# Kernel optimization log

Hardware: AMD Instinct MI355X
Metric: run time of the kernel (lower is better)

## Reference

```python
import jax, jax.numpy as jnp
import numpy as np

B, L, D, N_ORIG, GD, K_TARGET = 8, 512, 1024, 8192, 64, 256
_PI, _PJ = np.triu_indices(L, k=1)  # all global pairs i<j, shared across batch


def setup_inputs() -> dict:
    key = jax.random.key(0)
    k1, k2, k3 = jax.random.split(key, 3)
    x = jax.random.normal(k1, (B, L, D), jnp.float32)
    source = jax.random.uniform(k2, (B, L, N_ORIG), jnp.float32)
    W = jax.random.normal(k3, (GD, D), jnp.float32) * 0.02  # group_proj weight (out,in), no bias
    return {"x": x, "source": source, "W": W, "target_len": K_TARGET}


def _merge_single(x, s, W, r_step, pi, pj):
    # x: (S,D), s: (S,N). One greedy global merge step (r_step = S//2 >= r_total).
    S = x.shape[0]
    g = x @ W.T                                   # (S, GD)
    gn = jnp.linalg.norm(g, axis=-1)              # token weights (g.norm)
    gu = g / jnp.maximum(gn, 1e-12)[:, None]      # F.normalize(g, dim=-1)
    sim = (gu[pi] * gu[pj]).sum(-1)               # (P,) cosine sim of each pair
    # deterministic order: (-sim, i, j); lexsort's last key is primary
    order = jnp.lexsort((pj, pi, -sim))
    si = pi[order]
    sj = pj[order]

    # sequential greedy disjoint (mutual-exclusion) selection
    def body(carry, ij):
        partner, isj, cnt = carry
        i, j = ij
        used_i = (partner[i] >= 0) | isj[i]
        used_j = (partner[j] >= 0) | isj[j]
        sel = (~used_i) & (~used_j) & (cnt < r_step)
        partner = partner.at[i].set(jnp.where(sel, j, partner[i]))
        isj = isj.at[j].set(isj[j] | sel)
        return (partner, isj, cnt + sel.astype(jnp.int32)), None

    init = (jnp.full((S,), -1, jnp.int32), jnp.zeros((S,), bool), jnp.int32(0))
    (partner, isj, _), _ = jax.lax.scan(body, init, (si, sj))

    # kept tokens (everything not a merged-away j), in original order; greedy on a
    # complete graph always selects exactly r_step pairs, so K = S - r_step is static
    K = S - r_step
    keep = jnp.argsort(isj.astype(jnp.int32), stable=True)[:K]  # (K,)
    pk = partner[keep]
    has_p = pk >= 0
    pjx = jnp.where(has_p, pk, keep)  # safe partner index
    wi = gn[keep]
    wj = gn[pjx]
    tot = wi + wj + 1e-8
    xm = jnp.where(has_p[:, None], (wi[:, None] * x[keep] + wj[:, None] * x[pjx]) / tot[:, None], x[keep])
    sm = jnp.where(has_p[:, None], s[keep] + s[pjx], s[keep])
    return xm, sm


def reference(x, source, W, target_len):
    Bb, Ll, Dd = x.shape
    r_total = Ll - target_len
    if r_total <= 0:
        return x, source
    # with target_len = L//2, r_total <= floor(L/2): single greedy step (faithful)
    r_step = min(r_total, Ll // 2)
    pi = jnp.asarray(_PI, jnp.int32)
    pj = jnp.asarray(_PJ, jnp.int32)
    f = lambda xb, sb: _merge_single(xb, sb, W, r_step, pi, pj)
    return jax.vmap(f)(x, source)
```

## Files before the change

### kernel.cpp

```cpp
#include <hip/hip_runtime.h>

#define B_ 8
#define L_ 512
#define D_ 1024
#define N_ 8192
#define GD_ 64
#define K_ 256

__global__ __launch_bounds__(256) void wt_kernel(const float* __restrict__ W,
                                                 float* __restrict__ Wt) {
  int idx = blockIdx.x * 256 + threadIdx.x;
  int d = idx >> 6, g = idx & 63;
  Wt[idx] = W[(size_t)g * D_ + d];
}

__global__ __launch_bounds__(256) void gproj_kernel(const float* __restrict__ x,
                                                    const float* __restrict__ Wt,
                                                    float* __restrict__ gu,
                                                    float* __restrict__ gn) {
  const int KC = 128;
  __shared__ float xs[16][KC];
  __shared__ float wsT[GD_][KC + 4];
  int blk = blockIdx.x;
  int b = blk >> 5;
  int t0 = (blk & 31) * 16;
  int tid = threadIdx.x;
  int dg = tid & 15, tg = tid >> 4;
  const float* xb = x + ((size_t)b * L_ + t0) * D_;
  float ax[4] = {0, 0, 0, 0}, ay[4] = {0, 0, 0, 0};
  float az[4] = {0, 0, 0, 0}, aw[4] = {0, 0, 0, 0};
  for (int kc = 0; kc < D_; kc += KC) {
    for (int f = tid; f < 16 * KC / 4; f += 256) {
      int t = f >> 5, k4 = f & 31;
      *(float4*)&xs[t][k4 * 4] = *(const float4*)(xb + (size_t)t * D_ + kc + k4 * 4);
    }
    for (int f = tid; f < GD_ * KC; f += 256) {
      int kk = f >> 6, d = f & 63;
      wsT[d][kk] = Wt[(size_t)(kc + kk) * GD_ + d];
    }
    __syncthreads();
#pragma unroll 4
    for (int kk = 0; kk < KC; kk += 4) {
      float4 xv = *(const float4*)&xs[tg][kk];
#pragma unroll
      for (int dd = 0; dd < 4; ++dd) {
        float4 wv = *(const float4*)&wsT[dg * 4 + dd][kk];
        ax[dd] += xv.x * wv.x;
        ay[dd] += xv.y * wv.y;
        az[dd] += xv.z * wv.z;
        aw[dd] += xv.w * wv.w;
      }
    }
    __syncthreads();
  }
  float g[4];
  double ss = 0.0;
#pragma unroll
  for (int dd = 0; dd < 4; ++dd) {
    g[dd] = (ax[dd] + ay[dd]) + (az[dd] + aw[dd]);
    ss += (double)g[dd] * (double)g[dd];
  }
#pragma unroll
  for (int off = 1; off < 16; off <<= 1) ss += __shfl_xor(ss, off);
  float gnv = (float)sqrt(ss);
  float dn = fmaxf(gnv, 1e-12f);
  int t = t0 + tg;
  if (dg == 0) gn[(size_t)b * L_ + t] = gnv;
  float* gup = gu + ((size_t)b * L_ + t) * GD_ + dg * 4;
#pragma unroll
  for (int dd = 0; dd < 4; ++dd) gup[dd] = g[dd] / dn;
}

__global__ __launch_bounds__(256) void sim_kernel(const float* __restrict__ gu,
                                                  float* __restrict__ simo) {
  __shared__ __align__(16) float A[32][65];
  __shared__ __align__(16) float BsT[64][36];
  int b = blockIdx.z;
  int i0 = blockIdx.y * 32, j0 = blockIdx.x * 32;
  const float* gb = gu + (size_t)b * L_ * GD_;
  int tid = threadIdx.x;
  for (int f = tid; f < 32 * GD_; f += 256) {
    int r = f >> 6, k = f & 63;
    A[r][k] = gb[(size_t)(i0 + r) * GD_ + k];
    BsT[k][r] = gb[(size_t)(j0 + r) * GD_ + k];
  }
  __syncthreads();
  int r = tid >> 3, c4 = (tid & 7) * 4;
  double a0 = 0, a1 = 0, a2 = 0, a3 = 0;
#pragma unroll 8
  for (int k = 0; k < GD_; ++k) {
    double a = (double)A[r][k];
    float4 bv = *(const float4*)&BsT[k][c4];
    a0 += a * (double)bv.x;
    a1 += a * (double)bv.y;
    a2 += a * (double)bv.z;
    a3 += a * (double)bv.w;
  }
  float4 o;
  o.x = (float)a0; o.y = (float)a1; o.z = (float)a2; o.w = (float)a3;
  *(float4*)(simo + (size_t)b * L_ * L_ + (size_t)(i0 + r) * L_ + (j0 + c4)) = o;
}

__global__ __launch_bounds__(256) void topk_kernel(const float* __restrict__ sim,
                                                   unsigned long long* __restrict__ cand) {
  int wid = blockIdx.x * 4 + (threadIdx.x >> 6);
  int b = wid >> 9;
  int a = wid & 511;
  int lane = threadIdx.x & 63;
  const float* row = sim + ((size_t)b * L_ + a) * L_;
  int c0 = lane * 8;
  float4 v0 = *(const float4*)(row + c0);
  float4 v1 = *(const float4*)(row + c0 + 4);
  float vv[8] = {v0.x, v0.y, v0.z, v0.w, v1.x, v1.y, v1.z, v1.w};
  unsigned long long k[8];
#pragma unroll
  for (int s = 0; s < 8; ++s) {
    int bb = c0 + s;
    if (bb == a) {
      k[s] = 0;
    } else {
      unsigned u = __float_as_uint(vv[s]);
      u = (u & 0x80000000u) ? ~u : (u | 0x80000000u);
      int i = a < bb ? a : bb, j = a < bb ? bb : a;
      k[s] = ((unsigned long long)u << 18) |
             (unsigned long long)(0x3FFFFu - (((unsigned)i << 9) | (unsigned)j));
    }
  }
  unsigned long long* out = cand + ((size_t)b * L_ + a) * 16;
#pragma unroll
  for (int pass = 0; pass < 16; ++pass) {
    unsigned long long m = k[0];
#pragma unroll
    for (int s = 1; s < 8; ++s) m = k[s] > m ? k[s] : m;
#pragma unroll
    for (int off = 32; off; off >>= 1) {
      unsigned long long o = __shfl_xor(m, off);
      if (o > m) m = o;
    }
#pragma unroll
    for (int s = 0; s < 8; ++s)
      if (k[s] == m) k[s] = 0;
    if (lane == 0) out[pass] = m;
  }
}

__global__ __launch_bounds__(512) void match_kernel(const float* __restrict__ sim,
                                                    const unsigned long long* __restrict__ cand,
                                                    int* __restrict__ keepI,
                                                    int* __restrict__ keepJ) {
  int b = blockIdx.x;
  const float* S = sim + (size_t)b * L_ * L_;
  const unsigned long long* C = cand + (size_t)b * L_ * 16;
  __shared__ unsigned long long bestkey[L_];
  __shared__ short partner[L_];
  __shared__ short liveList[L_], liveTmp[L_], rescanQ[L_];
  __shared__ unsigned char liveF[L_], needs[L_], head[L_];
  __shared__ int nLiveS, nLiveNew, nQ;
  int tid = threadIdx.x;
  int wave = tid >> 6, lane = tid & 63;
  if (tid < L_) {
    partner[tid] = -1;
    liveF[tid] = 1;
    needs[tid] = 1;
    head[tid] = 0;
    liveList[tid] = (short)tid;
    bestkey[tid] = 0ull;
  }
  if (tid == 0) nLiveS = L_;
  __syncthreads();
  for (int round = 0; round < 300; ++round) {
    int nLive = nLiveS;
    if (nLive == 0) break;
    if (tid == 0) nQ = 0;
    __syncthreads();
    for (int idx = tid; idx < nLive; idx += 512) {
      int a = liveList[idx];
      if (needs[a]) {
        int h = head[a];
        unsigned long long bk = 0ull;
        while (h < 16) {
          unsigned long long key = C[a * 16 + h];
          if (key) {
            unsigned pk = 0x3FFFFu - (unsigned)(key & 0x3FFFFull);
            int i = (int)(pk >> 9), j = (int)(pk & 511u);
            int p = (i == a) ? j : i;
            if (liveF[p]) { bk = key; break; }
          }
          ++h;
        }
        head[a] = (unsigned char)h;
        if (bk) {
          bestkey[a] = bk;
          needs[a] = 0;
        } else {
          int q = atomicAdd(&nQ, 1);
          rescanQ[q] = (short)a;
        }
      }
    }
    __syncthreads();
    int nq = nQ;
    for (int q = wave; q < nq; q += 8) {
      int a = rescanQ[q];
      unsigned long long mk = 0ull;
      for (int kk = lane; kk < nLive; kk += 64) {
        int bb = liveList[kk];
        if (bb != a) {
          float sv = S[(size_t)a * L_ + bb];
          unsigned u = __float_as_uint(sv);
          u = (u & 0x80000000u) ? ~u : (u | 0x80000000u);
          int i = a < bb ? a : bb, j = a < bb ? bb : a;
          unsigned long long key =
              ((unsigned long long)u << 18) |
              (unsigned long long)(0x3FFFFu - (((unsigned)i << 9) | (unsigned)j));
          if (key > mk) mk = key;
        }
      }
#pragma unroll
      for (int off = 32; off; off >>= 1) {
        unsigned long long o = __shfl_xor(mk, off);
        if (o > mk) mk = o;
      }
      if (lane == 0) {
        bestkey[a] = mk;
        needs[a] = 0;
      }
    }
    __syncthreads();
    for (int idx = tid; idx < nLive; idx += 512) {
      int a = liveList[idx];
      unsigned pk = 0x3FFFFu - (unsigned)(bestkey[a] & 0x3FFFFull);
      int i = (int)(pk >> 9), j = (int)(pk & 511u);
      int p = (i == a) ? j : i;
      unsigned pk2 = 0x3FFFFu - (unsigned)(bestkey[p] & 0x3FFFFull);
      int i2 = (int)(pk2 >> 9), j2 = (int)(pk2 & 511u);
      int p2 = (i2 == p) ? j2 : i2;
      if (p2 == a) {
        partner[a] = (short)p;
        liveF[a] = 0;
      }
    }
    __syncthreads();
    if (tid == 0) nLiveNew = 0;
    __syncthreads();
    for (int idx = tid; idx < nLive; idx += 512) {
      int a = liveList[idx];
      if (liveF[a]) {
        unsigned pk = 0x3FFFFu - (unsigned)(bestkey[a] & 0x3FFFFull);
        int i = (int)(pk >> 9), j = (int)(pk & 511u);
        int p = (i == a) ? j : i;
        if (!liveF[p]) needs[a] = 1;
        int pos = atomicAdd(&nLiveNew, 1);
        liveTmp[pos] = (short)a;
      }
    }
    __syncthreads();
    int nNew = nLiveNew;
    for (int idx = tid; idx < nNew; idx += 512) liveList[idx] = liveTmp[idx];
    if (tid == 0) nLiveS = nNew;
    __syncthreads();
  }
  if (wave == 0) {
    int base = 0;
    for (int c = 0; c < 8; ++c) {
      int a = c * 64 + lane;
      bool kept = partner[a] > a;
      unsigned long long m = __ballot(kept);
      int pos = base + (int)__popcll(m & ((1ull << lane) - 1ull));
      if (kept) {
        keepI[b * K_ + pos] = a;
        keepJ[b * K_ + pos] = partner[a];
      }
      base += (int)__popcll(m);
    }
  }
}

__global__ __launch_bounds__(256) void mergex_kernel(const float* __restrict__ x,
                                                     const float* __restrict__ gn,
                                                     const int* __restrict__ keepI,
                                                     const int* __restrict__ keepJ,
                                                     float* __restrict__ out) {
  int row = blockIdx.x;
  int b = row >> 8;
  int i = keepI[row], j = keepJ[row];
  float wi = gn[(size_t)b * L_ + i], wj = gn[(size_t)b * L_ + j];
  float tot = wi + wj + 1e-8f;
  const float4* xi = (const float4*)(x + ((size_t)b * L_ + i) * D_);
  const float4* xj = (const float4*)(x + ((size_t)b * L_ + j) * D_);
  float4* o = (float4*)(out + (size_t)row * D_);
  int t = threadIdx.x;
  float4 a = xi[t], c = xj[t];
  float4 r;
  r.x = (wi * a.x + wj * c.x) / tot;
  r.y = (wi * a.y + wj * c.y) / tot;
  r.z = (wi * a.z + wj * c.z) / tot;
  r.w = (wi * a.w + wj * c.w) / tot;
  o[t] = r;
}

__global__ __launch_bounds__(256) void merges_kernel(const float* __restrict__ s,
                                                     const int* __restrict__ keepI,
                                                     const int* __restrict__ keepJ,
                                                     float* __restrict__ out) {
  int row = blockIdx.x;
  int b = row >> 8;
  int i = keepI[row], j = keepJ[row];
  const float4* si = (const float4*)(s + ((size_t)b * L_ + i) * N_);
  const float4* sj = (const float4*)(s + ((size_t)b * L_ + j) * N_);
  float4* o = (float4*)(out + (size_t)row * N_);
  for (int t = threadIdx.x; t < N_ / 4; t += 256) {
    float4 a = si[t], c = sj[t];
    float4 r;
    r.x = a.x + c.x;
    r.y = a.y + c.y;
    r.z = a.z + c.z;
    r.w = a.w + c.w;
    o[t] = r;
  }
}

extern "C" void kernel_launch(void* const* d_in, const int* in_sizes, int n_in,
                              void* d_out, int out_size, void* d_ws, size_t ws_size,
                              hipStream_t stream) {
  (void)in_sizes; (void)n_in; (void)out_size; (void)ws_size;
  const float* x = (const float*)d_in[0];
  const float* src = (const float*)d_in[1];
  const float* W = (const float*)d_in[2];

  float* ws = (float*)d_ws;
  float* Wt = ws;
  float* gu = Wt + 65536;
  float* gn = gu + (size_t)B_ * L_ * GD_;
  float* sim = gn + (size_t)B_ * L_;
  int* keepI = (int*)(sim + (size_t)B_ * L_ * L_);
  int* keepJ = keepI + B_ * K_;
  unsigned long long* cand = (unsigned long long*)(keepJ + B_ * K_);

  float* xm = (float*)d_out;
  float* sm = xm + (size_t)B_ * K_ * D_;

  wt_kernel<<<256, 256, 0, stream>>>(W, Wt);
  gproj_kernel<<<256, 256, 0, stream>>>(x, Wt, gu, gn);
  sim_kernel<<<dim3(16, 16, 8), 256, 0, stream>>>(gu, sim);
  topk_kernel<<<1024, 256, 0, stream>>>(sim, cand);
  match_kernel<<<B_, 512, 0, stream>>>(sim, cand, keepI, keepJ);
  mergex_kernel<<<B_ * K_, 256, 0, stream>>>(x, gn, keepI, keepJ, xm);
  merges_kernel<<<B_ * K_, 256, 0, stream>>>(src, keepI, keepJ, sm);
}
```

Baseline: 355.1 us.

## Drop W transpose kernel, fuse merge kernels, stage candidates in LDS

Removes the separate W-transpose kernel and loads W rows directly with float4 in gproj, which now uses 128 threads each computing two tokens. The sim kernel keeps the A row in registers instead of LDS. The match kernel copies the candidate lists into shared memory, ping-pongs the live lists to drop a copy loop, and removes two barriers per round. The x and source merge kernels are fused into one launch. Together these aim to cut launch count, global-memory latency in the serial matching loop, and synchronisation, at the cost of more LDS in match_kernel and fewer threads in gproj.

```diff
diff --git a/kernel.cpp b/kernel.cpp
--- a/kernel.cpp
+++ b/kernel.cpp
@@ -7,89 +7,97 @@
 #define GD_ 64
 #define K_ 256
 
-__global__ __launch_bounds__(256) void wt_kernel(const float* __restrict__ W,
-                                                 float* __restrict__ Wt) {
-  int idx = blockIdx.x * 256 + threadIdx.x;
-  int d = idx >> 6, g = idx & 63;
-  Wt[idx] = W[(size_t)g * D_ + d];
-}
-
-__global__ __launch_bounds__(256) void gproj_kernel(const float* __restrict__ x,
-                                                    const float* __restrict__ Wt,
+__global__ __launch_bounds__(128) void gproj_kernel(const float* __restrict__ x,
+                                                    const float* __restrict__ W,
                                                     float* __restrict__ gu,
                                                     float* __restrict__ gn) {
   const int KC = 128;
-  __shared__ float xs[16][KC];
-  __shared__ float wsT[GD_][KC + 4];
+  __shared__ __align__(16) float xs[16][KC];
+  __shared__ __align__(16) float wsT[GD_][KC + 4];
   int blk = blockIdx.x;
   int b = blk >> 5;
   int t0 = (blk & 31) * 16;
   int tid = threadIdx.x;
   int dg = tid & 15, tg = tid >> 4;
   const float* xb = x + ((size_t)b * L_ + t0) * D_;
-  float ax[4] = {0, 0, 0, 0}, ay[4] = {0, 0, 0, 0};
-  float az[4] = {0, 0, 0, 0}, aw[4] = {0, 0, 0, 0};
+  float acc[2][4][4];
+#pragma unroll
+  for (int tk = 0; tk < 2; ++tk)
+#pragma unroll
+    for (int dd = 0; dd < 4; ++dd)
+#pragma unroll
+      for (int c = 0; c < 4; ++c) acc[tk][dd][c] = 0.f;
   for (int kc = 0; kc < D_; kc += KC) {
-    for (int f = tid; f < 16 * KC / 4; f += 256) {
+    for (int f = tid; f < 16 * KC / 4; f += 128) {
       int t = f >> 5, k4 = f & 31;
       *(float4*)&xs[t][k4 * 4] = *(const float4*)(xb + (size_t)t * D_ + kc + k4 * 4);
     }
-    for (int f = tid; f < GD_ * KC; f += 256) {
-      int kk = f >> 6, d = f & 63;
-      wsT[d][kk] = Wt[(size_t)(kc + kk) * GD_ + d];
+    for (int f = tid; f < GD_ * KC / 4; f += 128) {
+      int d = f >> 5, k4 = f & 31;
+      *(float4*)&wsT[d][k4 * 4] = *(const float4*)(W + (size_t)d * D_ + kc + k4 * 4);
     }
     __syncthreads();
 #pragma unroll 4
     for (int kk = 0; kk < KC; kk += 4) {
-      float4 xv = *(const float4*)&xs[tg][kk];
+      float4 xv0 = *(const float4*)&xs[tg][kk];
+      float4 xv1 = *(const float4*)&xs[tg + 8][kk];
 #pragma unroll
       for (int dd = 0; dd < 4; ++dd) {
         float4 wv = *(const float4*)&wsT[dg * 4 + dd][kk];
-        ax[dd] += xv.x * wv.x;
-        ay[dd] += xv.y * wv.y;
-        az[dd] += xv.z * wv.z;
-        aw[dd] += xv.w * wv.w;
-      }
-    }
-    __syncthreads();
-  }
-  float g[4];
-  double ss = 0.0;
-#pragma unroll
-  for (int dd = 0; dd < 4; ++dd) {
-    g[dd] = (ax[dd] + ay[dd]) + (az[dd] + aw[dd]);
-    ss += (double)g[dd] * (double)g[dd];
-  }
-#pragma unroll
-  for (int off = 1; off < 16; off <<= 1) ss += __shfl_xor(ss, off);
-  float gnv = (float)sqrt(ss);
-  float dn = fmaxf(gnv, 1e-12f);
-  int t = t0 + tg;
-  if (dg == 0) gn[(size_t)b * L_ + t] = gnv;
-  float* gup = gu + ((size_t)b * L_ + t) * GD_ + dg * 4;
-#pragma unroll
-  for (int dd = 0; dd < 4; ++dd) gup[dd] = g[dd] / dn;
+        acc[0][dd][0] += xv0.x * wv.x;
+        acc[0][dd][1] += xv0.y * wv.y;
+        acc[0][dd][2] += xv0.z * wv.z;
+        acc[0][dd][3] += xv0.w * wv.w;
+        acc[1][dd][0] += xv1.x * wv.x;
+        acc[1][dd][1] += xv1.y * wv.y;
+        acc[1][dd][2] += xv1.z * wv.z;
+        acc[1][dd][3] += xv1.w * wv.w;
+      }
+    }
+    __syncthreads();
+  }
+#pragma unroll
+  for (int tk = 0; tk < 2; ++tk) {
+    float g[4];
+    double ss = 0.0;
+#pragma unroll
+    for (int dd = 0; dd < 4; ++dd) {
+      g[dd] = (acc[tk][dd][0] + acc[tk][dd][1]) + (acc[tk][dd][2] + acc[tk][dd][3]);
+      ss += (double)g[dd] * (double)g[dd];
+    }
+#pragma unroll
+    for (int off = 1; off < 16; off <<= 1) ss += __shfl_xor(ss, off);
+    float gnv = (float)sqrt(ss);
+    float dn = fmaxf(gnv, 1e-12f);
+    int t = t0 + tg + tk * 8;
+    if (dg == 0) gn[(size_t)b * L_ + t] = gnv;
+    float* gup = gu + ((size_t)b * L_ + t) * GD_ + dg * 4;
+#pragma unroll
+    for (int dd = 0; dd < 4; ++dd) gup[dd] = g[dd] / dn;
+  }
 }
 
 __global__ __launch_bounds__(256) void sim_kernel(const float* __restrict__ gu,
                                                   float* __restrict__ simo) {
-  __shared__ __align__(16) float A[32][65];
-  __shared__ __align__(16) float BsT[64][36];
+  __shared__ __align__(16) float BsT[GD_][36];
   int b = blockIdx.z;
   int i0 = blockIdx.y * 32, j0 = blockIdx.x * 32;
   const float* gb = gu + (size_t)b * L_ * GD_;
   int tid = threadIdx.x;
   for (int f = tid; f < 32 * GD_; f += 256) {
     int r = f >> 6, k = f & 63;
-    A[r][k] = gb[(size_t)(i0 + r) * GD_ + k];
     BsT[k][r] = gb[(size_t)(j0 + r) * GD_ + k];
   }
+  int r = tid >> 3, c4 = (tid & 7) * 4;
+  float af[GD_];
+  const float4* arow = (const float4*)(gb + (size_t)(i0 + r) * GD_);
+#pragma unroll
+  for (int q = 0; q < 16; ++q) *(float4*)&af[q * 4] = arow[q];
   __syncthreads();
-  int r = tid >> 3, c4 = (tid & 7) * 4;
   double a0 = 0, a1 = 0, a2 = 0, a3 = 0;
-#pragma unroll 8
+#pragma unroll
   for (int k = 0; k < GD_; ++k) {
-    double a = (double)A[r][k];
+    double a = (double)af[k];
     float4 bv = *(const float4*)&BsT[k][c4];
     a0 += a * (double)bv.x;
     a1 += a * (double)bv.y;
@@ -151,35 +159,41 @@
   int b = blockIdx.x;
   const float* S = sim + (size_t)b * L_ * L_;
   const unsigned long long* C = cand + (size_t)b * L_ * 16;
+  __shared__ unsigned long long candL[L_][16];
   __shared__ unsigned long long bestkey[L_];
   __shared__ short partner[L_];
-  __shared__ short liveList[L_], liveTmp[L_], rescanQ[L_];
+  __shared__ short liveA[L_], liveB[L_], rescanQ[L_];
   __shared__ unsigned char liveF[L_], needs[L_], head[L_];
-  __shared__ int nLiveS, nLiveNew, nQ;
+  __shared__ int nLiveNew, nQ;
   int tid = threadIdx.x;
   int wave = tid >> 6, lane = tid & 63;
+  for (int f = tid; f < L_ * 8; f += 512)
+    ((ulonglong2*)candL)[f] = ((const ulonglong2*)C)[f];
   if (tid < L_) {
     partner[tid] = -1;
     liveF[tid] = 1;
     needs[tid] = 1;
     head[tid] = 0;
-    liveList[tid] = (short)tid;
+    liveA[tid] = (short)tid;
     bestkey[tid] = 0ull;
   }
-  if (tid == 0) nLiveS = L_;
+  if (tid == 0) {
+    nLiveNew = L_;
+    nQ = 0;
+  }
   __syncthreads();
   for (int round = 0; round < 300; ++round) {
-    int nLive = nLiveS;
+    int nLive = nLiveNew;
     if (nLive == 0) break;
-    if (tid == 0) nQ = 0;
-    __syncthreads();
+    short* cur = (round & 1) ? liveB : liveA;
+    short* nxt = (round & 1) ? liveA : liveB;
     for (int idx = tid; idx < nLive; idx += 512) {
-      int a = liveList[idx];
+      int a = cur[idx];
       if (needs[a]) {
         int h = head[a];
         unsigned long long bk = 0ull;
         while (h < 16) {
-          unsigned long long key = C[a * 16 + h];
+          unsigned long long key = candL[a][h];
           if (key) {
             unsigned pk = 0x3FFFFu - (unsigned)(key & 0x3FFFFull);
             int i = (int)(pk >> 9), j = (int)(pk & 511u);
@@ -204,7 +218,7 @@
       int a = rescanQ[q];
       unsigned long long mk = 0ull;
       for (int kk = lane; kk < nLive; kk += 64) {
-        int bb = liveList[kk];
+        int bb = cur[kk];
         if (bb != a) {
           float sv = S[(size_t)a * L_ + bb];
           unsigned u = __float_as_uint(sv);
@@ -226,9 +240,10 @@
         needs[a] = 0;
       }
     }
+    if (tid == 0) nLiveNew = 0;
     __syncthreads();
     for (int idx = tid; idx < nLive; idx += 512) {
-      int a = liveList[idx];
+      int a = cur[idx];
       unsigned pk = 0x3FFFFu - (unsigned)(bestkey[a] & 0x3FFFFull);
       int i = (int)(pk >> 9), j = (int)(pk & 511u);
       int p = (i == a) ? j : i;
@@ -241,23 +256,18 @@
       }
     }
     __syncthreads();
-    if (tid == 0) nLiveNew = 0;
-    __syncthreads();
     for (int idx = tid; idx < nLive; idx += 512) {
-      int a = liveList[idx];
+      int a = cur[idx];
       if (liveF[a]) {
         unsigned pk = 0x3FFFFu - (unsigned)(bestkey[a] & 0x3FFFFull);
         int i = (int)(pk >> 9), j = (int)(pk & 511u);
         int p = (i == a) ? j : i;
         if (!liveF[p]) needs[a] = 1;
         int pos = atomicAdd(&nLiveNew, 1);
-        liveTmp[pos] = (short)a;
-      }
-    }
-    __syncthreads();
-    int nNew = nLiveNew;
-    for (int idx = tid; idx < nNew; idx += 512) liveList[idx] = liveTmp[idx];
-    if (tid == 0) nLiveS = nNew;
+        nxt[pos] = (short)a;
+      }
+    }
+    if (tid == 0) nQ = 0;
     __syncthreads();
   }
   if (wave == 0) {
@@ -276,47 +286,44 @@
   }
 }
 
-__global__ __launch_bounds__(256) void mergex_kernel(const float* __restrict__ x,
-                                                     const float* __restrict__ gn,
-                                                     const int* __restrict__ keepI,
-                                                     const int* __restrict__ keepJ,
-                                                     float* __restrict__ out) {
+__global__ __launch_bounds__(256) void merge_kernel(const float* __restrict__ x,
+                                                    const float* __restrict__ s,
+                                                    const float* __restrict__ gn,
+                                                    const int* __restrict__ keepI,
+                                                    const int* __restrict__ keepJ,
+                                                    float* __restrict__ xm,
+                                                    float* __restrict__ sm) {
   int row = blockIdx.x;
   int b = row >> 8;
   int i = keepI[row], j = keepJ[row];
   float wi = gn[(size_t)b * L_ + i], wj = gn[(size_t)b * L_ + j];
   float tot = wi + wj + 1e-8f;
-  const float4* xi = (const float4*)(x + ((size_t)b * L_ + i) * D_);
-  const float4* xj = (const float4*)(x + ((size_t)b * L_ + j) * D_);
-  float4* o = (float4*)(out + (size_t)row * D_);
   int t = threadIdx.x;
-  float4 a = xi[t], c = xj[t];
-  float4 r;
-  r.x = (wi * a.x + wj * c.x) / tot;
-  r.y = (wi * a.y + wj * c.y) / tot;
-  r.z = (wi * a.z + wj * c.z) / tot;
-  r.w = (wi * a.w + wj * c.w) / tot;
-  o[t] = r;
-}
-
-__global__ __launch_bounds__(256) void merges_kernel(const float* __restrict__ s,
-                                                     const int* __restrict__ keepI,
-                                                     const int* __restrict__ keepJ,
-                                                     float* __restrict__ out) {
-  int row = blockIdx.x;
-  int b = row >> 8;
-  int i = keepI[row], j = keepJ[row];
-  const float4* si = (const float4*)(s + ((size_t)b * L_ + i) * N_);
-  const float4* sj = (const float4*)(s + ((size_t)b * L_ + j) * N_);
-  float4* o = (float4*)(out + (size_t)row * N_);
-  for (int t = threadIdx.x; t < N_ / 4; t += 256) {
-    float4 a = si[t], c = sj[t];
+  {
+    const float4* xi = (const float4*)(x + ((size_t)b * L_ + i) * D_);
+    const float4* xj = (const float4*)(x + ((size_t)b * L_ + j) * D_);
+    float4* o = (float4*)(xm + (size_t)row * D_);
+    float4 a = xi[t], c = xj[t];
     float4 r;
-    r.x = a.x + c.x;
-    r.y = a.y + c.y;
-    r.z = a.z + c.z;
-    r.w = a.w + c.w;
+    r.x = (wi * a.x + wj * c.x) / tot;
+    r.y = (wi * a.y + wj * c.y) / tot;
+    r.z = (wi * a.z + wj * c.z) / tot;
+    r.w = (wi * a.w + wj * c.w) / tot;
     o[t] = r;
+  }
+  {
+    const float4* si = (const float4*)(s + ((size_t)b * L_ + i) * N_);
+    const float4* sj = (const float4*)(s + ((size_t)b * L_ + j) * N_);
+    float4* o = (float4*)(sm + (size_t)row * N_);
+    for (int tt = t; tt < N_ / 4; tt += 256) {
+      float4 a = si[tt], c = sj[tt];
+      float4 r;
+      r.x = a.x + c.x;
+      r.y = a.y + c.y;
+      r.z = a.z + c.z;
+      r.w = a.w + c.w;
+      o[tt] = r;
+    }
   }
 }
 
@@ -329,8 +336,7 @@
   const float* W = (const float*)d_in[2];
 
   float* ws = (float*)d_ws;
-  float* Wt = ws;
-  float* gu = Wt + 65536;
+  float* gu = ws;
   float* gn = gu + (size_t)B_ * L_ * GD_;
   float* sim = gn + (size_t)B_ * L_;
   int* keepI = (int*)(sim + (size_t)B_ * L_ * L_);
@@ -340,11 +346,9 @@
   float* xm = (float*)d_out;
   float* sm = xm + (size_t)B_ * K_ * D_;
 
-  wt_kernel<<<256, 256, 0, stream>>>(W, Wt);
-  gproj_kernel<<<256, 256, 0, stream>>>(x, Wt, gu, gn);
+  gproj_kernel<<<256, 128, 0, stream>>>(x, W, gu, gn);
   sim_kernel<<<dim3(16, 16, 8), 256, 0, stream>>>(gu, sim);
   topk_kernel<<<1024, 256, 0, stream>>>(sim, cand);
   match_kernel<<<B_, 512, 0, stream>>>(sim, cand, keepI, keepJ);
-  mergex_kernel<<<B_ * K_, 256, 0, stream>>>(x, gn, keepI, keepJ, xm);
-  merges_kernel<<<B_ * K_, 256, 0, stream>>>(src, keepI, keepJ, sm);
-}
+  merge_kernel<<<B_ * K_, 256, 0, stream>>>(x, src, gn, keepI, keepJ, xm, sm);
+}
```

New measurement: 383.3 us. 1.08x slower.
